# Optimization experiments

Hardware: AMD Instinct MI355X
Metric: run time of the kernel (lower is better)

## Reference

```python
import jax, jax.numpy as jnp
import numpy as np

N = 240000
B = 2
GRID = (480, 360, 32)
NUM_CLASS = 20
IGNORE_LABEL = 0
MINB = np.array([0.0, -np.pi, -4.0], np.float32)
MAXB = np.array([50.0, np.pi, 2.0], np.float32)
EPS = 1e-5


def setup_inputs() -> dict:
    key = jax.random.key(0)
    ks = jax.random.split(key, 32)
    d = {}
    d['pt_fea'] = jax.random.normal(ks[0], (N, 6), jnp.float32)
    # cylindrical coords (rho, phi, z) uniformly inside the volume
    u = jax.random.uniform(ks[1], (N, 3), jnp.float32)
    d['xyz'] = u * jnp.asarray(MAXB - MINB) + jnp.asarray(MINB)
    d['batch_idx'] = jnp.sort(jax.random.randint(ks[2], (N,), 0, B)).astype(jnp.int64)
    d['pt_lab'] = jax.random.randint(ks[3], (N,), 0, NUM_CLASS).astype(jnp.int64)
    d['shuffled_ind'] = jnp.arange(N, dtype=jnp.int64)  # identity perm (deterministic)
    i = 4
    for name, c in [('bn0', 9), ('bn1', 64), ('bn2', 128), ('bn3', 256)]:
        d[name + '_g'] = jax.random.uniform(ks[i], (c,), jnp.float32, 0.5, 1.5); i += 1
        d[name + '_b'] = jax.random.normal(ks[i], (c,), jnp.float32) * 0.1; i += 1
        d[name + '_m'] = jax.random.normal(ks[i], (c,), jnp.float32) * 0.1; i += 1
        d[name + '_v'] = jax.random.uniform(ks[i], (c,), jnp.float32, 0.5, 1.5); i += 1
    for name, (fi, fo) in [('1', (9, 64)), ('2', (64, 128)), ('3', (128, 256)), ('4', (256, 256))]:
        d['w' + name] = jax.random.normal(ks[i], (fi, fo), jnp.float32) / np.sqrt(fi); i += 1
        d['b' + name] = jax.random.normal(ks[i], (fo,), jnp.float32) * 0.01; i += 1
    d['wc'] = jax.random.normal(ks[i], (256, 16), jnp.float32) / 16.0; i += 1
    d['bc'] = jax.random.normal(ks[i], (16,), jnp.float32) * 0.01
    return d


def _bn(x, g, b, m, v):
    return (x - m) * (g * jax.lax.rsqrt(v + EPS)) + b


def _ppmodel(feat, bn0_g, bn0_b, bn0_m, bn0_v, w1, b1, bn1_g, bn1_b, bn1_m, bn1_v,
             w2, b2, bn2_g, bn2_b, bn2_m, bn2_v, w3, b3, bn3_g, bn3_b, bn3_m, bn3_v, w4, b4):
    x = _bn(feat, bn0_g, bn0_b, bn0_m, bn0_v)
    x = jax.nn.relu(_bn(x @ w1 + b1, bn1_g, bn1_b, bn1_m, bn1_v))
    x = jax.nn.relu(_bn(x @ w2 + b2, bn2_g, bn2_b, bn2_m, bn2_v))
    x = jax.nn.relu(_bn(x @ w3 + b3, bn3_g, bn3_b, bn3_m, bn3_v))
    return x @ w4 + b4  # [N, 256]


def reference(pt_fea, xyz, batch_idx, pt_lab, shuffled_ind,
              bn0_g, bn0_b, bn0_m, bn0_v, w1, b1, bn1_g, bn1_b, bn1_m, bn1_v,
              w2, b2, bn2_g, bn2_b, bn2_m, bn2_v, w3, b3, bn3_g, bn3_b, bn3_m, bn3_v,
              w4, b4, wc, bc):
    minb = jnp.asarray(MINB)
    maxb = jnp.asarray(MAXB)
    grid = jnp.asarray(np.array(GRID, np.float32))
    intervals = (maxb - minb) / (grid - 1.0)

    clamped = jnp.clip(xyz, minb, maxb)
    ind = jnp.floor((clamped - minb) / intervals).astype(jnp.int32)  # [N,3]
    voxel_centers = (ind.astype(jnp.float32) + 0.5) * intervals + minb
    rel_xyz = xyz - voxel_centers
    feat = jnp.concatenate([rel_xyz, pt_fea], axis=1)  # [N,9]

    bi = batch_idx.astype(jnp.int32)
    counts = jnp.full((B,) + GRID + (NUM_CLASS,), IGNORE_LABEL, jnp.int32)
    counts = counts.at[bi, ind[:, 0], ind[:, 1], ind[:, 2], pt_lab].add(1)
    voxel_labels = jnp.argmax(counts, axis=-1).astype(jnp.int32)  # [B,480,360,32]

    feat = feat[shuffled_ind]

    flat = ((bi.astype(jnp.int64) * GRID[0] + ind[:, 0]) * GRID[1] + ind[:, 1]) * GRID[2] + ind[:, 2]
    unq, unq_inv = jnp.unique(flat, size=N, fill_value=-1, return_inverse=True)
    unq_inv = unq_inv.reshape(-1)

    processed = _ppmodel(feat, bn0_g, bn0_b, bn0_m, bn0_v, w1, b1, bn1_g, bn1_b, bn1_m, bn1_v,
                         w2, b2, bn2_g, bn2_b, bn2_m, bn2_v, w3, b3, bn3_g, bn3_b, bn3_m, bn3_v, w4, b4)
    pooled = jax.ops.segment_max(processed, unq_inv, num_segments=N)
    seg_cnt = jax.ops.segment_sum(jnp.ones((N,), jnp.float32), unq_inv, num_segments=N)
    pooled = jnp.where(seg_cnt[:, None] > 0, pooled, 0.0)  # zero out empty (padded) segments

    processed_pooled = jax.nn.relu(pooled @ wc + bc)  # fea_compression

    cat_pt_ind = jnp.concatenate([batch_idx[:, None], ind.astype(jnp.int64)], axis=1)
    return (unq, processed_pooled, voxel_labels, cat_pt_ind)
```

## Files before the change

kernel.cpp:

```cpp
#include <hip/hip_runtime.h>
#include <stdint.h>

#define N_PTS 240000
#define NV    11059200
#define NWORDS 172800
#define NB_PT 938
#define NB_WORD 675
#define NBLK_MLP 3750

typedef __bf16 bf16x8 __attribute__((ext_vector_type(8)));
typedef short  short8 __attribute__((ext_vector_type(8)));
typedef float  f32x4  __attribute__((ext_vector_type(4)));

__device__ __forceinline__ unsigned short f2bf(float f) {
  unsigned u = __builtin_bit_cast(unsigned, f);
  return (unsigned short)((u + 0x7FFFu + ((u >> 16) & 1u)) >> 16);
}
__device__ __forceinline__ float bf2f(unsigned short h) {
  unsigned u = ((unsigned)h) << 16;
  return __builtin_bit_cast(float, u);
}

__global__ void prep_kernel(
    const float* __restrict__ bng0, const float* __restrict__ bnb0, const float* __restrict__ bnm0, const float* __restrict__ bnv0,
    const float* __restrict__ bng1, const float* __restrict__ bnb1, const float* __restrict__ bnm1, const float* __restrict__ bnv1,
    const float* __restrict__ bng2, const float* __restrict__ bnb2, const float* __restrict__ bnm2, const float* __restrict__ bnv2,
    const float* __restrict__ bng3, const float* __restrict__ bnb3, const float* __restrict__ bnm3, const float* __restrict__ bnv3,
    const float* __restrict__ w1, const float* __restrict__ b1,
    const float* __restrict__ w2, const float* __restrict__ b2,
    const float* __restrict__ w3, const float* __restrict__ b3,
    const float* __restrict__ w4, const float* __restrict__ wc,
    float* __restrict__ s0, float* __restrict__ t0, float* __restrict__ w1e, float* __restrict__ be1,
    float* __restrict__ be2, float* __restrict__ be3,
    unsigned short* __restrict__ w2t, unsigned short* __restrict__ w3t, unsigned short* __restrict__ w4t,
    unsigned short* __restrict__ wct)
{
  const int id = blockIdx.x * 256 + threadIdx.x;
  { int c = id >> 8, k = id & 255; w4t[c * 256 + k] = f2bf(w4[k * 256 + c]); }
  if (id < 32768) { int c = id >> 7, k = id & 127;
    float s = bng3[c] * rsqrtf(bnv3[c] + 1e-5f);
    w3t[c * 128 + k] = f2bf(w3[k * 256 + c] * s); }
  if (id < 8192) { int c = id >> 6, k = id & 63;
    float s = bng2[c] * rsqrtf(bnv2[c] + 1e-5f);
    w2t[c * 64 + k] = f2bf(w2[k * 128 + c] * s); }
  if (id < 4096) { int c = id >> 8, k = id & 255;
    wct[c * 256 + k] = f2bf(wc[k * 16 + c]); }
  if (id < 576) { int k = id / 64, c = id % 64;
    float s = bng1[c] * rsqrtf(bnv1[c] + 1e-5f);
    w1e[k * 64 + c] = w1[k * 64 + c] * s; }
  if (id < 64)  { float s = bng1[id] * rsqrtf(bnv1[id] + 1e-5f); be1[id] = (b1[id] - bnm1[id]) * s + bnb1[id]; }
  if (id < 128) { float s = bng2[id] * rsqrtf(bnv2[id] + 1e-5f); be2[id] = (b2[id] - bnm2[id]) * s + bnb2[id]; }
  if (id < 256) { float s = bng3[id] * rsqrtf(bnv3[id] + 1e-5f); be3[id] = (b3[id] - bnm3[id]) * s + bnb3[id]; }
  if (id < 9)   { float s = bng0[id] * rsqrtf(bnv0[id] + 1e-5f); s0[id] = s; t0[id] = bnb0[id] - bnm0[id] * s; }
}

__global__ void vox_kernel(
    const float* __restrict__ xyz, const int* __restrict__ bidx,
    unsigned* __restrict__ flatkeys, unsigned long long* __restrict__ bitmap,
    float* __restrict__ out_cat)
{
  const int j = blockIdx.x * 256 + threadIdx.x;
  if (j >= N_PTS) return;
  const float PI_F = 3.14159265358979323846f;
  const float minb[3] = {0.0f, -PI_F, -4.0f};
  const float maxb[3] = {50.0f, PI_F, 2.0f};
  const float gm1[3]  = {479.0f, 359.0f, 31.0f};
  int ind[3];
  #pragma unroll
  for (int d = 0; d < 3; ++d) {
    float itv = (maxb[d] - minb[d]) / gm1[d];
    float x  = xyz[(size_t)j * 3 + d];
    float cl = fminf(fmaxf(x, minb[d]), maxb[d]);
    ind[d] = (int)floorf((cl - minb[d]) / itv);
  }
  const int bi = bidx[j];
  const unsigned flat = ((unsigned)(bi * 480 + ind[0]) * 360u + (unsigned)ind[1]) * 32u + (unsigned)ind[2];
  flatkeys[j] = flat;
  atomicOr(&bitmap[flat >> 6], 1ull << (flat & 63u));
  float* oc = out_cat + (size_t)j * 4;
  oc[0] = (float)bi; oc[1] = (float)ind[0]; oc[2] = (float)ind[1]; oc[3] = (float)ind[2];
}

__global__ void reduce_words(const unsigned long long* __restrict__ bm, unsigned* __restrict__ bsums) {
  __shared__ unsigned sh[256];
  const int w = blockIdx.x * 256 + threadIdx.x;
  sh[threadIdx.x] = (unsigned)__popcll(bm[w]);
  __syncthreads();
  for (int s = 128; s > 0; s >>= 1) { if (threadIdx.x < s) sh[threadIdx.x] += sh[threadIdx.x + s]; __syncthreads(); }
  if (threadIdx.x == 0) bsums[blockIdx.x] = sh[0];
}

__global__ void scan_small(unsigned* __restrict__ d, int n) {
  __shared__ unsigned sh[1024];
  const int t = threadIdx.x;
  unsigned own = (t < n) ? d[t] : 0u;
  sh[t] = own; __syncthreads();
  for (int off = 1; off < 1024; off <<= 1) {
    unsigned v = (t >= off) ? sh[t - off] : 0u;
    __syncthreads(); sh[t] += v; __syncthreads();
  }
  if (t < n) d[t] = sh[t] - own;
}

__global__ void scatter_unq(const unsigned long long* __restrict__ bm, const unsigned* __restrict__ bsums,
                            unsigned* __restrict__ wordpref, unsigned* __restrict__ unqvals,
                            float* __restrict__ out_unq) {
  __shared__ unsigned sh[256];
  const int t = threadIdx.x;
  const int w = blockIdx.x * 256 + t;
  unsigned long long word = bm[w];
  unsigned own = (unsigned)__popcll(word);
  sh[t] = own; __syncthreads();
  for (int off = 1; off < 256; off <<= 1) {
    unsigned v = (t >= off) ? sh[t - off] : 0u;
    __syncthreads(); sh[t] += v; __syncthreads();
  }
  unsigned r = bsums[blockIdx.x] + sh[t] - own;
  wordpref[w] = r;
  while (word) {
    int b = __builtin_ctzll(word);
    unsigned id = (unsigned)w * 64u + (unsigned)b;
    unqvals[r] = id;
    out_unq[r] = (float)id;
    ++r;
    word &= word - 1;
  }
}

__global__ void inv_kernel(const unsigned* __restrict__ flatkeys, const unsigned long long* __restrict__ bm,
                           const unsigned* __restrict__ wordpref, const int* __restrict__ ptlab,
                           unsigned* __restrict__ unq_inv, unsigned* __restrict__ cnt, unsigned* __restrict__ counts) {
  const int j = blockIdx.x * 256 + threadIdx.x;
  if (j >= N_PTS) return;
  const unsigned f = flatkeys[j];
  const unsigned w = f >> 6, b = f & 63u;
  const unsigned r = wordpref[w] + (unsigned)__popcll(bm[w] & ((1ull << b) - 1ull));
  unq_inv[j] = r;
  atomicAdd(&cnt[r], 1u);
  const unsigned lab = (unsigned)ptlab[j];
  atomicAdd(&counts[(size_t)r * 10 + (lab >> 1)], 1u << ((lab & 1u) * 16));
}

__global__ void reduce_cnt(const unsigned* __restrict__ cnt, unsigned* __restrict__ bsums) {
  __shared__ unsigned sh[256];
  const int j = blockIdx.x * 256 + threadIdx.x;
  sh[threadIdx.x] = (j < N_PTS) ? cnt[j] : 0u;
  __syncthreads();
  for (int s = 128; s > 0; s >>= 1) { if (threadIdx.x < s) sh[threadIdx.x] += sh[threadIdx.x + s]; __syncthreads(); }
  if (threadIdx.x == 0) bsums[blockIdx.x] = sh[0];
}
__global__ void scan_cnt(const unsigned* __restrict__ cnt, const unsigned* __restrict__ bsums,
                         unsigned* __restrict__ off, unsigned* __restrict__ cur) {
  __shared__ unsigned sh[256];
  const int t = threadIdx.x;
  const int j = blockIdx.x * 256 + t;
  unsigned own = (j < N_PTS) ? cnt[j] : 0u;
  sh[t] = own; __syncthreads();
  for (int o = 1; o < 256; o <<= 1) {
    unsigned v = (t >= o) ? sh[t - o] : 0u;
    __syncthreads(); sh[t] += v; __syncthreads();
  }
  if (j < N_PTS) { unsigned e = bsums[blockIdx.x] + sh[t] - own; off[j] = e; cur[j] = e; }
}
__global__ void plist_kernel(const unsigned* __restrict__ unq_inv, unsigned* __restrict__ cur,
                             unsigned* __restrict__ plist) {
  const int j = blockIdx.x * 256 + threadIdx.x;
  if (j >= N_PTS) return;
  plist[atomicAdd(&cur[unq_inv[j]], 1u)] = (unsigned)j;
}

__global__ void labels_kernel(const unsigned* __restrict__ cnt, const unsigned* __restrict__ counts,
                              const unsigned* __restrict__ unqvals, const float* __restrict__ bc,
                              float* __restrict__ out_lab, float* __restrict__ out_pooled) {
  const int u = blockIdx.x * 256 + threadIdx.x;
  if (u >= N_PTS) return;
  if (cnt[u] == 0) {
    #pragma unroll
    for (int c = 0; c < 16; ++c) out_pooled[(size_t)u * 16 + c] = fmaxf(bc[c], 0.f);
    return;
  }
  const unsigned* c = counts + (size_t)u * 10;
  int best = 0; unsigned bv = c[0] & 0xFFFFu;
  #pragma unroll
  for (int l = 1; l < 20; ++l) {
    unsigned v = (c[l >> 1] >> ((l & 1) * 16)) & 0xFFFFu;
    if (v > bv) { bv = v; best = l; }
  }
  out_lab[unqvals[u]] = (float)best;
}

__global__ void fill_unq_kernel(float* __restrict__ out_unq) {
  const int j = blockIdx.x * 256 + threadIdx.x;
  if (j < N_PTS) out_unq[j] = -1.0f;
}

template<int K, int C, int PIN, int POUT, bool RELU>
__device__ __forceinline__ void gemm_stage(
    const unsigned short* __restrict__ Wt,
    const float* __restrict__ bias,
    const unsigned short* actIn,
    unsigned short* actOut,
    int tid)
{
  constexpr int NT = C / 64;
  const int wave = tid >> 6, lane = tid & 63;
  const int l15  = lane & 15, quad = lane >> 4;
  f32x4 acc[4][NT];
  #pragma unroll
  for (int mt = 0; mt < 4; ++mt)
    #pragma unroll
    for (int nt = 0; nt < NT; ++nt) acc[mt][nt] = (f32x4){0.f, 0.f, 0.f, 0.f};
  const unsigned short* wp[NT];
  #pragma unroll
  for (int nt = 0; nt < NT; ++nt)
    wp[nt] = Wt + (size_t)(wave * 16 * NT + nt * 16 + l15) * K + quad * 8;
  #pragma unroll
  for (int kc = 0; kc < K; kc += 32) {
    bf16x8 b[NT];
    #pragma unroll
    for (int nt = 0; nt < NT; ++nt)
      b[nt] = __builtin_bit_cast(bf16x8, *(const short8*)(wp[nt] + kc));
    #pragma unroll
    for (int mt = 0; mt < 4; ++mt) {
      bf16x8 a = __builtin_bit_cast(bf16x8, *(const short8*)&actIn[(mt * 16 + l15) * PIN + kc + quad * 8]);
      #pragma unroll
      for (int nt = 0; nt < NT; ++nt)
        acc[mt][nt] = __builtin_amdgcn_mfma_f32_16x16x32_bf16(a, b[nt], acc[mt][nt], 0, 0, 0);
    }
  }
  __syncthreads();
  #pragma unroll
  for (int mt = 0; mt < 4; ++mt)
    #pragma unroll
    for (int nt = 0; nt < NT; ++nt) {
      const int c0 = wave * 16 * NT + nt * 16 + l15;
      const float bs = bias[c0];
      #pragma unroll
      for (int r = 0; r < 4; ++r) {
        const int rl = mt * 16 + quad * 4 + r;
        float y = acc[mt][nt][r] + bs;
        if (RELU) y = fmaxf(y, 0.f);
        actOut[rl * POUT + c0] = f2bf(y);
      }
    }
  __syncthreads();
}

#define PA 264
#define PB 136

__global__ __launch_bounds__(256, 3) void mlp_pool_kernel(
    const float* __restrict__ ptfea, const float* __restrict__ xyz, const int* __restrict__ shuf,
    const unsigned* __restrict__ plist, const unsigned* __restrict__ unq_inv,
    const unsigned* __restrict__ offv, const unsigned* __restrict__ cnt,
    const float* __restrict__ s0, const float* __restrict__ t0,
    const float* __restrict__ w1e, const float* __restrict__ be1,
    const unsigned short* __restrict__ w2t, const float* __restrict__ be2,
    const unsigned short* __restrict__ w3t, const float* __restrict__ be3,
    const unsigned short* __restrict__ w4t, const float* __restrict__ b4,
    const unsigned short* __restrict__ wct, const float* __restrict__ bc,
    unsigned short* __restrict__ partials, float* __restrict__ out_pooled)
{
  __shared__ __align__(16) unsigned short bufA[64 * PA];
  __shared__ __align__(16) unsigned short bufB[64 * PB];
  __shared__ int segs[64];
  __shared__ int jrows[64];
  __shared__ int s_alast;
  __shared__ unsigned char s_lead[64], s_comp[64];
  const int tid  = threadIdx.x;
  const int row0 = blockIdx.x * 64;

  if (tid == 0) s_alast = 0;
  if (tid < 64) {
    int j = (int)plist[row0 + tid];
    jrows[tid] = j;
    segs[tid] = (int)unq_inv[j];
  }
  __syncthreads();

  {
    const int r = tid >> 2, part = tid & 3;
    const int sj = shuf[jrows[r]];
    const float PI_F = 3.14159265358979323846f;
    const float minb[3] = {0.0f, -PI_F, -4.0f};
    const float maxb[3] = {50.0f, PI_F, 2.0f};
    const float gm1[3]  = {479.0f, 359.0f, 31.0f};
    float x0[9];
    #pragma unroll
    for (int d = 0; d < 3; ++d) {
      float itv = (maxb[d] - minb[d]) / gm1[d];
      float x   = xyz[(size_t)sj * 3 + d];
      float cl  = fminf(fmaxf(x, minb[d]), maxb[d]);
      float fi  = floorf((cl - minb[d]) / itv);
      float center = (fi + 0.5f) * itv + minb[d];
      x0[d] = (x - center) * s0[d] + t0[d];
    }
    #pragma unroll
    for (int d = 0; d < 6; ++d) x0[3 + d] = ptfea[(size_t)sj * 6 + d] * s0[3 + d] + t0[3 + d];
    #pragma unroll
    for (int ci = 0; ci < 16; ++ci) {
      const int c = part * 16 + ci;
      float acc = be1[c];
      #pragma unroll
      for (int k = 0; k < 9; ++k) acc += x0[k] * w1e[k * 64 + c];
      bufA[r * PA + c] = f2bf(fmaxf(acc, 0.0f));
    }
  }
  __syncthreads();

  gemm_stage< 64, 128, PA, PB, true >(w2t, be2, bufA, bufB, tid);
  gemm_stage<128, 256, PB, PA, true >(w3t, be3, bufB, bufA, tid);
  gemm_stage<256, 256, PA, PA, false>(w4t, b4,  bufA, bufA, tid);

  if (tid < 64) {
    const int r = tid;
    bool lead = (r == 0) || (segs[r] != segs[r - 1]);
    s_lead[r] = lead ? 1 : 0;
    unsigned char comp = 0;
    if (lead) {
      atomicMax(&s_alast, r);
      int e = r + 1;
      while (e < 64 && segs[e] == segs[r]) ++e;
      const unsigned s = (unsigned)segs[r];
      comp = (offv[s] == (unsigned)(row0 + r) && offv[s] + cnt[s] == (unsigned)(row0 + e)) ? 1 : 0;
    }
    s_comp[r] = comp;
  }
  __syncthreads();

  {
    const int c = tid;
    float cur = bf2f(bufA[63 * PA + c]);
    for (int r = 62; r >= 0; --r) {
      float x = bf2f(bufA[r * PA + c]);
      cur = (segs[r] == segs[r + 1]) ? fmaxf(cur, x) : x;
      bufA[r * PA + c] = f2bf(cur);
    }
  }
  __syncthreads();

  {
    const int c = tid;
    const int alast = s_alast;
    const size_t b2 = (size_t)blockIdx.x * 2;
    if (!s_comp[0])     partials[b2 * 256 + c]       = bufA[0 * PA + c];
    if (!s_comp[alast]) partials[(b2 + 1) * 256 + c] = bufA[alast * PA + c];
  }

  {
    const int wave = tid >> 6, lane = tid & 63;
    const int l15 = lane & 15, quad = lane >> 4;
    const unsigned short* wp = wct + l15 * 256 + quad * 8;
    f32x4 acc = (f32x4){0.f, 0.f, 0.f, 0.f};
    #pragma unroll
    for (int kc = 0; kc < 256; kc += 32) {
      bf16x8 a = __builtin_bit_cast(bf16x8, *(const short8*)&bufA[(wave * 16 + l15) * PA + kc + quad * 8]);
      bf16x8 b = __builtin_bit_cast(bf16x8, *(const short8*)(wp + kc));
      acc = __builtin_amdgcn_mfma_f32_16x16x32_bf16(a, b, acc, 0, 0, 0);
    }
    const float bcv = bc[l15];
    #pragma unroll
    for (int r = 0; r < 4; ++r) {
      const int rl = wave * 16 + quad * 4 + r;
      if (s_lead[rl] && s_comp[rl])
        out_pooled[(size_t)segs[rl] * 16 + l15] = fmaxf(acc[r] + bcv, 0.f);
    }
  }
}

__global__ __launch_bounds__(256) void merge_kernel(
    const unsigned* __restrict__ plist, const unsigned* __restrict__ unq_inv,
    const unsigned* __restrict__ offv, const unsigned* __restrict__ cnt,
    const unsigned short* __restrict__ partials,
    const float* __restrict__ wc, const float* __restrict__ bc,
    float* __restrict__ out_pooled)
{
  __shared__ float pooled[256];
  __shared__ float psum[256];
  const int b = blockIdx.x;
  const unsigned s = unq_inv[plist[(size_t)b * 64 + 63]];
  const unsigned o = offv[s], e = o + cnt[s];
  if ((o >> 6) != (unsigned)b) return;
  if (e <= (unsigned)(b + 1) * 64) return;
  const int B1 = (int)((e - 1) >> 6);
  const int c = threadIdx.x;
  float m = bf2f(partials[((size_t)2 * b + 1) * 256 + c]);
  for (int bb = b + 1; bb <= B1; ++bb)
    m = fmaxf(m, bf2f(partials[(size_t)2 * bb * 256 + c]));
  pooled[c] = m;
  __syncthreads();
  const int co = c & 15, kg = c >> 4;
  float p = 0.f;
  #pragma unroll
  for (int k = kg * 16; k < kg * 16 + 16; ++k) p += pooled[k] * wc[k * 16 + co];
  psum[c] = p;
  __syncthreads();
  if (c < 16) {
    float acc = bc[c];
    #pragma unroll
    for (int g = 0; g < 16; ++g) acc += psum[g * 16 + c];
    out_pooled[(size_t)s * 16 + c] = fmaxf(acc, 0.f);
  }
}

extern "C" void kernel_launch(void* const* d_in, const int* in_sizes, int n_in,
                              void* d_out, int out_size, void* d_ws, size_t ws_size,
                              hipStream_t stream)
{
  const float* pt_fea = (const float*)d_in[0];
  const float* xyz    = (const float*)d_in[1];
  const int*   bidx   = (const int*)d_in[2];
  const int*   ptlab  = (const int*)d_in[3];
  const int*   shuf   = (const int*)d_in[4];
  const float* bng0 = (const float*)d_in[5],  *bnb0 = (const float*)d_in[6],  *bnm0 = (const float*)d_in[7],  *bnv0 = (const float*)d_in[8];
  const float* bng1 = (const float*)d_in[9],  *bnb1 = (const float*)d_in[10], *bnm1 = (const float*)d_in[11], *bnv1 = (const float*)d_in[12];
  const float* bng2 = (const float*)d_in[13], *bnb2 = (const float*)d_in[14], *bnm2 = (const float*)d_in[15], *bnv2 = (const float*)d_in[16];
  const float* bng3 = (const float*)d_in[17], *bnb3 = (const float*)d_in[18], *bnm3 = (const float*)d_in[19], *bnv3 = (const float*)d_in[20];
  const float* w1 = (const float*)d_in[21], *b1 = (const float*)d_in[22];
  const float* w2 = (const float*)d_in[23], *b2 = (const float*)d_in[24];
  const float* w3 = (const float*)d_in[25], *b3 = (const float*)d_in[26];
  const float* w4 = (const float*)d_in[27], *b4 = (const float*)d_in[28];
  const float* wc = (const float*)d_in[29], *bc = (const float*)d_in[30];

  float* out        = (float*)d_out;
  float* out_unq    = out;
  float* out_pooled = out + 240000;
  float* out_lab    = out + 4080000;
  float* out_cat    = out + 15139200;

  char* wsb = (char*)d_ws;
  size_t o = 0;
  auto alloc = [&](size_t bytes) -> void* { void* p = wsb + o; o = (o + bytes + 255) & ~(size_t)255; return p; };
  float* s0  = (float*)alloc(9 * 4);
  float* t0  = (float*)alloc(9 * 4);
  float* w1e = (float*)alloc(576 * 4);
  float* be1 = (float*)alloc(64 * 4);
  float* be2 = (float*)alloc(128 * 4);
  float* be3 = (float*)alloc(256 * 4);
  unsigned short* w2t = (unsigned short*)alloc(8192 * 2);
  unsigned short* w3t = (unsigned short*)alloc(32768 * 2);
  unsigned short* w4t = (unsigned short*)alloc(65536 * 2);
  unsigned short* wct = (unsigned short*)alloc(4096 * 2);
  unsigned* flatkeys = (unsigned*)alloc((size_t)N_PTS * 4);
  unsigned* unq_inv  = (unsigned*)alloc((size_t)N_PTS * 4);
  unsigned* unqvals  = (unsigned*)alloc((size_t)N_PTS * 4);
  unsigned* cnt      = (unsigned*)alloc((size_t)N_PTS * 4);
  unsigned* offv     = (unsigned*)alloc((size_t)N_PTS * 4);
  unsigned* cur      = (unsigned*)alloc((size_t)N_PTS * 4);
  unsigned* plist    = (unsigned*)alloc((size_t)N_PTS * 4);
  unsigned long long* bitmap = (unsigned long long*)alloc((size_t)NWORDS * 8);
  unsigned* wordpref = (unsigned*)alloc((size_t)NWORDS * 4);
  unsigned* bsumA    = (unsigned*)alloc(NB_WORD * 4);
  unsigned* bsumB    = (unsigned*)alloc(NB_PT * 4);
  unsigned* counts   = (unsigned*)alloc((size_t)N_PTS * 10 * 4);
  unsigned short* partials = (unsigned short*)alloc((size_t)NBLK_MLP * 2 * 256 * 2);

  hipMemsetAsync(bitmap, 0, (size_t)NWORDS * 8, stream);
  hipMemsetAsync(cnt, 0, (size_t)N_PTS * 4, stream);
  hipMemsetAsync(counts, 0, (size_t)N_PTS * 10 * 4, stream);
  hipMemsetAsync(out_lab, 0, (size_t)NV * 4, stream);

  prep_kernel<<<256, 256, 0, stream>>>(bng0, bnb0, bnm0, bnv0, bng1, bnb1, bnm1, bnv1,
                                       bng2, bnb2, bnm2, bnv2, bng3, bnb3, bnm3, bnv3,
                                       w1, b1, w2, b2, w3, b3, w4, wc,
                                       s0, t0, w1e, be1, be2, be3, w2t, w3t, w4t, wct);
  fill_unq_kernel<<<NB_PT, 256, 0, stream>>>(out_unq);
  vox_kernel<<<NB_PT, 256, 0, stream>>>(xyz, bidx, flatkeys, bitmap, out_cat);
  reduce_words<<<NB_WORD, 256, 0, stream>>>(bitmap, bsumA);
  scan_small<<<1, 1024, 0, stream>>>(bsumA, NB_WORD);
  scatter_unq<<<NB_WORD, 256, 0, stream>>>(bitmap, bsumA, wordpref, unqvals, out_unq);
  inv_kernel<<<NB_PT, 256, 0, stream>>>(flatkeys, bitmap, wordpref, ptlab, unq_inv, cnt, counts);
  reduce_cnt<<<NB_PT, 256, 0, stream>>>(cnt, bsumB);
  scan_small<<<1, 1024, 0, stream>>>(bsumB, NB_PT);
  scan_cnt<<<NB_PT, 256, 0, stream>>>(cnt, bsumB, offv, cur);
  plist_kernel<<<NB_PT, 256, 0, stream>>>(unq_inv, cur, plist);
  labels_kernel<<<NB_PT, 256, 0, stream>>>(cnt, counts, unqvals, bc, out_lab, out_pooled);
  mlp_pool_kernel<<<NBLK_MLP, 256, 0, stream>>>(pt_fea, xyz, shuf, plist, unq_inv, offv, cnt,
                                                s0, t0, w1e, be1, w2t, be2, w3t, be3, w4t, b4,
                                                wct, bc, partials, out_pooled);
  merge_kernel<<<NBLK_MLP, 256, 0, stream>>>(plist, unq_inv, offv, cnt, partials, wc, bc, out_pooled);
}
```

Measured before the change: 397.2 us.

## Give each wave its own rows in MLP GEMMs, drop block barriers, fuse small kernels

The MLP GEMM stages now give each wave its own 16 rows and all output columns. The A fragments stay in registers and B is streamed from global memory, so the per-stage __syncthreads barriers go away and each wave works on its own rows independently. The fill_unq kernel is folded into vox_kernel and the plist and labels kernels are merged into one. The three workspace memsets become a single contiguous memset, and the segment-max scan now handles two columns per thread. In exchange, every wave re-reads all the weight rows instead of a quarter of them, which may raise L2/global traffic, and the in-place final stage now depends on each wave touching only its own rows.

```diff
diff --git a/kernel.cpp b/kernel.cpp
--- a/kernel.cpp
+++ b/kernel.cpp
@@ -57,10 +57,11 @@
 __global__ void vox_kernel(
     const float* __restrict__ xyz, const int* __restrict__ bidx,
     unsigned* __restrict__ flatkeys, unsigned long long* __restrict__ bitmap,
-    float* __restrict__ out_cat)
+    float* __restrict__ out_cat, float* __restrict__ out_unq)
 {
   const int j = blockIdx.x * 256 + threadIdx.x;
   if (j >= N_PTS) return;
+  out_unq[j] = -1.0f;
   const float PI_F = 3.14159265358979323846f;
   const float minb[3] = {0.0f, -PI_F, -4.0f};
   const float maxb[3] = {50.0f, PI_F, 2.0f};
@@ -162,18 +163,16 @@
   }
   if (j < N_PTS) { unsigned e = bsums[blockIdx.x] + sh[t] - own; off[j] = e; cur[j] = e; }
 }
-__global__ void plist_kernel(const unsigned* __restrict__ unq_inv, unsigned* __restrict__ cur,
-                             unsigned* __restrict__ plist) {
+
+__global__ void plist_labels_kernel(const unsigned* __restrict__ unq_inv, unsigned* __restrict__ cur,
+                                    unsigned* __restrict__ plist,
+                                    const unsigned* __restrict__ cnt, const unsigned* __restrict__ counts,
+                                    const unsigned* __restrict__ unqvals, const float* __restrict__ bc,
+                                    float* __restrict__ out_lab, float* __restrict__ out_pooled) {
   const int j = blockIdx.x * 256 + threadIdx.x;
   if (j >= N_PTS) return;
   plist[atomicAdd(&cur[unq_inv[j]], 1u)] = (unsigned)j;
-}
-
-__global__ void labels_kernel(const unsigned* __restrict__ cnt, const unsigned* __restrict__ counts,
-                              const unsigned* __restrict__ unqvals, const float* __restrict__ bc,
-                              float* __restrict__ out_lab, float* __restrict__ out_pooled) {
-  const int u = blockIdx.x * 256 + threadIdx.x;
-  if (u >= N_PTS) return;
+  const int u = j;
   if (cnt[u] == 0) {
     #pragma unroll
     for (int c = 0; c < 16; ++c) out_pooled[(size_t)u * 16 + c] = fmaxf(bc[c], 0.f);
@@ -189,61 +188,38 @@
   out_lab[unqvals[u]] = (float)best;
 }
 
-__global__ void fill_unq_kernel(float* __restrict__ out_unq) {
-  const int j = blockIdx.x * 256 + threadIdx.x;
-  if (j < N_PTS) out_unq[j] = -1.0f;
-}
-
 template<int K, int C, int PIN, int POUT, bool RELU>
-__device__ __forceinline__ void gemm_stage(
+__device__ __forceinline__ void gemm_stage_w(
     const unsigned short* __restrict__ Wt,
     const float* __restrict__ bias,
     const unsigned short* actIn,
     unsigned short* actOut,
-    int tid)
-{
-  constexpr int NT = C / 64;
-  const int wave = tid >> 6, lane = tid & 63;
-  const int l15  = lane & 15, quad = lane >> 4;
-  f32x4 acc[4][NT];
+    int wave, int lane)
+{
+  constexpr int KC = K / 32;
+  constexpr int NT = C / 16;
+  const int l15 = lane & 15, quad = lane >> 4;
+  bf16x8 a[KC];
   #pragma unroll
-  for (int mt = 0; mt < 4; ++mt)
-    #pragma unroll
-    for (int nt = 0; nt < NT; ++nt) acc[mt][nt] = (f32x4){0.f, 0.f, 0.f, 0.f};
-  const unsigned short* wp[NT];
+  for (int kc = 0; kc < KC; ++kc)
+    a[kc] = __builtin_bit_cast(bf16x8, *(const short8*)&actIn[(wave * 16 + l15) * PIN + kc * 32 + quad * 8]);
+  const unsigned short* wp = Wt + (size_t)l15 * K + quad * 8;
   #pragma unroll
-  for (int nt = 0; nt < NT; ++nt)
-    wp[nt] = Wt + (size_t)(wave * 16 * NT + nt * 16 + l15) * K + quad * 8;
-  #pragma unroll
-  for (int kc = 0; kc < K; kc += 32) {
-    bf16x8 b[NT];
-    #pragma unroll
-    for (int nt = 0; nt < NT; ++nt)
-      b[nt] = __builtin_bit_cast(bf16x8, *(const short8*)(wp[nt] + kc));
-    #pragma unroll
-    for (int mt = 0; mt < 4; ++mt) {
-      bf16x8 a = __builtin_bit_cast(bf16x8, *(const short8*)&actIn[(mt * 16 + l15) * PIN + kc + quad * 8]);
-      #pragma unroll
-      for (int nt = 0; nt < NT; ++nt)
-        acc[mt][nt] = __builtin_amdgcn_mfma_f32_16x16x32_bf16(a, b[nt], acc[mt][nt], 0, 0, 0);
-    }
-  }
-  __syncthreads();
-  #pragma unroll
-  for (int mt = 0; mt < 4; ++mt)
-    #pragma unroll
-    for (int nt = 0; nt < NT; ++nt) {
-      const int c0 = wave * 16 * NT + nt * 16 + l15;
-      const float bs = bias[c0];
-      #pragma unroll
-      for (int r = 0; r < 4; ++r) {
-        const int rl = mt * 16 + quad * 4 + r;
-        float y = acc[mt][nt][r] + bs;
-        if (RELU) y = fmaxf(y, 0.f);
-        actOut[rl * POUT + c0] = f2bf(y);
-      }
-    }
-  __syncthreads();
+  for (int nt = 0; nt < NT; ++nt) {
+    f32x4 acc = (f32x4){0.f, 0.f, 0.f, 0.f};
+    #pragma unroll
+    for (int kc = 0; kc < KC; ++kc) {
+      bf16x8 b = __builtin_bit_cast(bf16x8, *(const short8*)(wp + (size_t)nt * 16 * K + kc * 32));
+      acc = __builtin_amdgcn_mfma_f32_16x16x32_bf16(a[kc], b, acc, 0, 0, 0);
+    }
+    const float bs = bias[nt * 16 + l15];
+    #pragma unroll
+    for (int r = 0; r < 4; ++r) {
+      float y = acc[r] + bs;
+      if (RELU) y = fmaxf(y, 0.f);
+      actOut[(wave * 16 + quad * 4 + r) * POUT + nt * 16 + l15] = f2bf(y);
+    }
+  }
 }
 
 #define PA 264
@@ -268,18 +244,19 @@
   __shared__ int s_alast;
   __shared__ unsigned char s_lead[64], s_comp[64];
   const int tid  = threadIdx.x;
+  const int wave = tid >> 6, lane = tid & 63;
   const int row0 = blockIdx.x * 64;
 
   if (tid == 0) s_alast = 0;
-  if (tid < 64) {
-    int j = (int)plist[row0 + tid];
-    jrows[tid] = j;
-    segs[tid] = (int)unq_inv[j];
-  }
-  __syncthreads();
+  if (lane < 16) {
+    const int r = wave * 16 + lane;
+    int j = (int)plist[row0 + r];
+    jrows[r] = j;
+    segs[r] = (int)unq_inv[j];
+  }
 
   {
-    const int r = tid >> 2, part = tid & 3;
+    const int r = wave * 16 + (lane >> 2), part = lane & 3;
     const int sj = shuf[jrows[r]];
     const float PI_F = 3.14159265358979323846f;
     const float minb[3] = {0.0f, -PI_F, -4.0f};
@@ -306,11 +283,12 @@
       bufA[r * PA + c] = f2bf(fmaxf(acc, 0.0f));
     }
   }
-  __syncthreads();
-
-  gemm_stage< 64, 128, PA, PB, true >(w2t, be2, bufA, bufB, tid);
-  gemm_stage<128, 256, PB, PA, true >(w3t, be3, bufB, bufA, tid);
-  gemm_stage<256, 256, PA, PA, false>(w4t, b4,  bufA, bufA, tid);
+
+  gemm_stage_w< 64, 128, PA, PB, true >(w2t, be2, bufA, bufB, wave, lane);
+  gemm_stage_w<128, 256, PB, PA, true >(w3t, be3, bufB, bufA, wave, lane);
+  gemm_stage_w<256, 256, PA, PA, false>(w4t, b4,  bufA, bufA, wave, lane);
+
+  __syncthreads();
 
   if (tid < 64) {
     const int r = tid;
@@ -326,15 +304,19 @@
     }
     s_comp[r] = comp;
   }
-  __syncthreads();
-
-  {
-    const int c = tid;
-    float cur = bf2f(bufA[63 * PA + c]);
+  if (tid >= 128) {
+    const int c2 = (tid - 128) * 2;
+    unsigned v = *(const unsigned*)&bufA[63 * PA + c2];
+    float cl = bf2f((unsigned short)(v & 0xFFFFu));
+    float ch = bf2f((unsigned short)(v >> 16));
     for (int r = 62; r >= 0; --r) {
-      float x = bf2f(bufA[r * PA + c]);
-      cur = (segs[r] == segs[r + 1]) ? fmaxf(cur, x) : x;
-      bufA[r * PA + c] = f2bf(cur);
+      unsigned x = *(const unsigned*)&bufA[r * PA + c2];
+      float xl = bf2f((unsigned short)(x & 0xFFFFu));
+      float xh = bf2f((unsigned short)(x >> 16));
+      const bool same = (segs[r] == segs[r + 1]);
+      cl = same ? fmaxf(cl, xl) : xl;
+      ch = same ? fmaxf(ch, xh) : xh;
+      *(unsigned*)&bufA[r * PA + c2] = (unsigned)f2bf(cl) | ((unsigned)f2bf(ch) << 16);
     }
   }
   __syncthreads();
@@ -348,7 +330,6 @@
   }
 
   {
-    const int wave = tid >> 6, lane = tid & 63;
     const int l15 = lane & 15, quad = lane >> 4;
     const unsigned short* wp = wct + l15 * 256 + quad * 8;
     f32x4 acc = (f32x4){0.f, 0.f, 0.f, 0.f};
@@ -431,6 +412,10 @@
   char* wsb = (char*)d_ws;
   size_t o = 0;
   auto alloc = [&](size_t bytes) -> void* { void* p = wsb + o; o = (o + bytes + 255) & ~(size_t)255; return p; };
+  unsigned long long* bitmap = (unsigned long long*)alloc((size_t)NWORDS * 8);
+  unsigned* cnt      = (unsigned*)alloc((size_t)N_PTS * 4);
+  unsigned* counts   = (unsigned*)alloc((size_t)N_PTS * 10 * 4);
+  const size_t zero_bytes = o;
   float* s0  = (float*)alloc(9 * 4);
   float* t0  = (float*)alloc(9 * 4);
   float* w1e = (float*)alloc(576 * 4);
@@ -444,28 +429,22 @@
   unsigned* flatkeys = (unsigned*)alloc((size_t)N_PTS * 4);
   unsigned* unq_inv  = (unsigned*)alloc((size_t)N_PTS * 4);
   unsigned* unqvals  = (unsigned*)alloc((size_t)N_PTS * 4);
-  unsigned* cnt      = (unsigned*)alloc((size_t)N_PTS * 4);
   unsigned* offv     = (unsigned*)alloc((size_t)N_PTS * 4);
   unsigned* cur      = (unsigned*)alloc((size_t)N_PTS * 4);
   unsigned* plist    = (unsigned*)alloc((size_t)N_PTS * 4);
-  unsigned long long* bitmap = (unsigned long long*)alloc((size_t)NWORDS * 8);
   unsigned* wordpref = (unsigned*)alloc((size_t)NWORDS * 4);
   unsigned* bsumA    = (unsigned*)alloc(NB_WORD * 4);
   unsigned* bsumB    = (unsigned*)alloc(NB_PT * 4);
-  unsigned* counts   = (unsigned*)alloc((size_t)N_PTS * 10 * 4);
   unsigned short* partials = (unsigned short*)alloc((size_t)NBLK_MLP * 2 * 256 * 2);
 
-  hipMemsetAsync(bitmap, 0, (size_t)NWORDS * 8, stream);
-  hipMemsetAsync(cnt, 0, (size_t)N_PTS * 4, stream);
-  hipMemsetAsync(counts, 0, (size_t)N_PTS * 10 * 4, stream);
+  hipMemsetAsync(bitmap, 0, zero_bytes, stream);
   hipMemsetAsync(out_lab, 0, (size_t)NV * 4, stream);
 
   prep_kernel<<<256, 256, 0, stream>>>(bng0, bnb0, bnm0, bnv0, bng1, bnb1, bnm1, bnv1,
                                        bng2, bnb2, bnm2, bnv2, bng3, bnb3, bnm3, bnv3,
                                        w1, b1, w2, b2, w3, b3, w4, wc,
                                        s0, t0, w1e, be1, be2, be3, w2t, w3t, w4t, wct);
-  fill_unq_kernel<<<NB_PT, 256, 0, stream>>>(out_unq);
-  vox_kernel<<<NB_PT, 256, 0, stream>>>(xyz, bidx, flatkeys, bitmap, out_cat);
+  vox_kernel<<<NB_PT, 256, 0, stream>>>(xyz, bidx, flatkeys, bitmap, out_cat, out_unq);
   reduce_words<<<NB_WORD, 256, 0, stream>>>(bitmap, bsumA);
   scan_small<<<1, 1024, 0, stream>>>(bsumA, NB_WORD);
   scatter_unq<<<NB_WORD, 256, 0, stream>>>(bitmap, bsumA, wordpref, unqvals, out_unq);
@@ -473,8 +452,8 @@
   reduce_cnt<<<NB_PT, 256, 0, stream>>>(cnt, bsumB);
   scan_small<<<1, 1024, 0, stream>>>(bsumB, NB_PT);
   scan_cnt<<<NB_PT, 256, 0, stream>>>(cnt, bsumB, offv, cur);
-  plist_kernel<<<NB_PT, 256, 0, stream>>>(unq_inv, cur, plist);
-  labels_kernel<<<NB_PT, 256, 0, stream>>>(cnt, counts, unqvals, bc, out_lab, out_pooled);
+  plist_labels_kernel<<<NB_PT, 256, 0, stream>>>(unq_inv, cur, plist, cnt, counts, unqvals, bc,
+                                                 out_lab, out_pooled);
   mlp_pool_kernel<<<NBLK_MLP, 256, 0, stream>>>(pt_fea, xyz, shuf, plist, unq_inv, offv, cnt,
                                                 s0, t0, w1e, be1, w2t, be2, w3t, be3, w4t, b4,
                                                 wct, bc, partials, out_pooled);
```

Result: slower. 612.5 us (+54.2%).
